# Optimization experiments

Measured on AMD Instinct MI355X. Metric: run time of the kernel, lower is better.

Reference implementation:

```python
import jax, jax.numpy as jnp
import numpy as np

N_NODES = 200000  # num_users + num_items
N_EDGES = 500000
LATENT = 64
N_LAYERS = 3
NEG_SLOPE = 0.01  # F.leaky_relu default
EPS = 1e-16       # PyG geo_softmax denominator epsilon


def setup_inputs() -> dict:
    key = jax.random.key(0)
    k1, k2, k3, k4, k5 = jax.random.split(key, 5)
    edge_index = jax.random.randint(k1, (2, N_EDGES), 0, N_NODES, dtype=jnp.int64 if jax.config.jax_enable_x64 else jnp.int32)
    edge_attrs = jax.random.normal(k2, (N_EDGES, 2), dtype=jnp.float32)
    emb = jax.random.normal(k3, (N_NODES, LATENT), dtype=jnp.float32)
    # per-layer attention params, shape [L, heads=1 -> squeezed, in_channels]
    a_att_w = jax.random.normal(k4, (N_LAYERS, LATENT), dtype=jnp.float32) * 0.1
    r_att_w = jax.random.normal(k5, (N_LAYERS, LATENT), dtype=jnp.float32) * 0.1
    return {"edge_index": edge_index, "edge_attrs": edge_attrs, "emb": emb,
            "a_att_w": a_att_w, "r_att_w": r_att_w}


def _segment_softmax(scores, dst, num_nodes):
    # scores: [E, D] softmax over edges grouped by destination node (PyG geo_softmax)
    m = jax.ops.segment_max(scores, dst, num_segments=num_nodes)  # [N, D]
    m = jnp.where(jnp.isfinite(m), m, 0.0)  # nodes without incoming edges
    w = jnp.exp(scores - m[dst])
    den = jax.ops.segment_sum(w, dst, num_segments=num_nodes)     # [N, D]
    return w / (den[dst] + EPS)


def reference(edge_index, edge_attrs, emb, a_att_w, r_att_w):
    src, dst = edge_index[0], edge_index[1]
    n = emb.shape[0]
    # symmetric degree normalization (degree of destination endpoints)
    deg = jax.ops.segment_sum(jnp.ones_like(dst, dtype=emb.dtype), dst, num_segments=n)
    dinv = jnp.where(deg > 0, deg ** -0.5, 0.0)
    norm = (dinv[src] * dinv[dst])[:, None]  # [E, 1]

    a_e = edge_attrs[:, 0:1]  # [E, 1]
    r_e = edge_attrs[:, 1:2]

    x = emb
    acc = emb  # layer-0 embedding
    for l in range(N_LAYERS):
        scores = (jax.nn.leaky_relu(a_e * a_att_w[l], NEG_SLOPE)
                  + jax.nn.leaky_relu(r_e * r_att_w[l], NEG_SLOPE))  # [E, D]
        attn = _segment_softmax(scores, dst, n)                       # [E, D]
        msg = norm * attn * x[src]                                    # gather + weight
        x = jax.ops.segment_sum(msg, dst, num_segments=n)             # scatter-add
        acc = acc + x
    out = acc / (N_LAYERS + 1)  # mean over layer embeddings
    return out
```

## Files before the change

### kernel.cpp

```cpp
#include <hip/hip_runtime.h>

#define BLK 256
#define LBLK 256
#define CH 1024

__device__ __forceinline__ unsigned short f2bf(float f) {
    unsigned u = __float_as_uint(f);
    u += 0x7FFFu + ((u >> 16) & 1u);
    return (unsigned short)(u >> 16);
}
__device__ __forceinline__ float bf2f(unsigned short h) {
    return __uint_as_float((unsigned)h << 16);
}
__device__ __forceinline__ float4 unpack4(ushort4 h) {
    return make_float4(bf2f(h.x), bf2f(h.y), bf2f(h.z), bf2f(h.w));
}
__device__ __forceinline__ ushort4 pack4(float4 f) {
    ushort4 h; h.x = f2bf(f.x); h.y = f2bf(f.y); h.z = f2bf(f.z); h.w = f2bf(f.w);
    return h;
}
__device__ __forceinline__ float4 unpack4u(uint2 u) {
    return make_float4(__uint_as_float(u.x << 16), __uint_as_float(u.x & 0xffff0000u),
                       __uint_as_float(u.y << 16), __uint_as_float(u.y & 0xffff0000u));
}
__device__ __forceinline__ unsigned pack2(float lo, float hi) {
    return (unsigned)f2bf(lo) | ((unsigned)f2bf(hi) << 16);
}


__global__ void k_deg(const int* __restrict__ dst, int* __restrict__ deg,
                      int* __restrict__ rank, int E) {
    int e = blockIdx.x * blockDim.x + threadIdx.x;
    if (e < E) rank[e] = atomicAdd(&deg[dst[e]], 1);
}

__global__ void k_scan1(const int* __restrict__ deg, int* __restrict__ partials, int N) {
    __shared__ int sm[BLK];
    int i0 = blockIdx.x * CH + threadIdx.x * 4;
    int s = 0;
    if (i0 + 3 < N) {
        int4 v = *(const int4*)(deg + i0);
        s = (v.x + v.y) + (v.z + v.w);
    } else {
        for (int k = 0; k < 4; ++k) if (i0 + k < N) s += deg[i0 + k];
    }
    sm[threadIdx.x] = s;
    __syncthreads();
    for (int off = BLK / 2; off > 0; off >>= 1) {
        if (threadIdx.x < off) sm[threadIdx.x] += sm[threadIdx.x + off];
        __syncthreads();
    }
    if (threadIdx.x == 0) partials[blockIdx.x] = sm[0];
}

__global__ void k_scan2(const int* __restrict__ deg, const int* __restrict__ partials,
                        int* __restrict__ row_off, int N, int E, int nb) {
    __shared__ int sp[BLK];
    __shared__ int sm[BLK];
    int b = blockIdx.x, t = threadIdx.x;
    sp[t] = (t < nb) ? partials[t] : 0;
    __syncthreads();
    for (int off = 1; off < BLK; off <<= 1) {
        int add = (t >= off) ? sp[t - off] : 0;
        __syncthreads();
        sp[t] += add;
        __syncthreads();
    }
    int base = (b == 0) ? 0 : sp[b - 1];
    if (b == 0 && t == 0) row_off[N] = E;
    int i0 = b * CH + t * 4;
    int v0 = 0, v1 = 0, v2 = 0, v3 = 0;
    if (i0 + 3 < N) {
        int4 v = *(const int4*)(deg + i0);
        v0 = v.x; v1 = v.y; v2 = v.z; v3 = v.w;
    } else {
        if (i0     < N) v0 = deg[i0];
        if (i0 + 1 < N) v1 = deg[i0 + 1];
        if (i0 + 2 < N) v2 = deg[i0 + 2];
    }
    int tot = (v0 + v1) + (v2 + v3);
    sm[t] = tot;
    __syncthreads();
    for (int off = 1; off < BLK; off <<= 1) {
        int add = (t >= off) ? sm[t - off] : 0;
        __syncthreads();
        sm[t] += add;
        __syncthreads();
    }
    int excl = base + sm[t] - tot;
    int4 r;
    r.x = excl;
    r.y = excl + v0;
    r.z = excl + v0 + v1;
    r.w = excl + v0 + v1 + v2;
    if (i0 + 3 < N) {
        *(int4*)(row_off + i0) = r;
    } else {
        if (i0     < N) row_off[i0]     = r.x;
        if (i0 + 1 < N) row_off[i0 + 1] = r.y;
        if (i0 + 2 < N) row_off[i0 + 2] = r.z;
    }
}

__global__ void k_convfill(const int* __restrict__ src, const int* __restrict__ dst,
                           const float2* __restrict__ attrs, const int* __restrict__ row_off,
                           const int* __restrict__ rank, const int* __restrict__ deg,
                           uint2* __restrict__ csr, const float4* __restrict__ emb4,
                           ushort4* __restrict__ embs, int E, int N16, int gF) {
    int b = blockIdx.x;
    if (b < gF) {
        int e = b * BLK + threadIdx.x;
        if (e >= E) return;
        int pos = row_off[dst[e]] + rank[e];
        float2 ar = attrs[e];
        csr[pos] = make_uint2((unsigned)src[e],
                              (unsigned)f2bf(ar.x) | ((unsigned)f2bf(ar.y) << 16));
    } else {
        int i = (b - gF) * BLK + threadIdx.x;
        if (i >= N16) return;
        int d = deg[i >> 4];
        float dinv = (d > 0) ? rsqrtf((float)d) : 0.0f;
        float4 e = emb4[i];
        embs[i] = pack4(make_float4(dinv * e.x, dinv * e.y, dinv * e.z, dinv * e.w));
    }
}


__device__ __forceinline__ float lrelu(float x) { return fmaxf(x, 0.01f * x); }

__device__ __forceinline__ void edge_w8(unsigned ar,
                                        const float4& awl, const float4& awh,
                                        const float4& rwl, const float4& rwh,
                                        float4& wl, float4& wh) {
    float a = bf2f((unsigned short)(ar & 0xffffu));
    float r = bf2f((unsigned short)(ar >> 16));
    wl.x = __expf(lrelu(a * awl.x) + lrelu(r * rwl.x));
    wl.y = __expf(lrelu(a * awl.y) + lrelu(r * rwl.y));
    wl.z = __expf(lrelu(a * awl.z) + lrelu(r * rwl.z));
    wl.w = __expf(lrelu(a * awl.w) + lrelu(r * rwl.w));
    wh.x = __expf(lrelu(a * awh.x) + lrelu(r * rwh.x));
    wh.y = __expf(lrelu(a * awh.y) + lrelu(r * rwh.y));
    wh.z = __expf(lrelu(a * awh.z) + lrelu(r * rwh.z));
    wh.w = __expf(lrelu(a * awh.w) + lrelu(r * rwh.w));
}

__device__ __forceinline__ void acc4u(float4& num, float4& den,
                                      const float4& w, uint2 xu, float g) {
    float4 x = unpack4u(xu);
    den.x += g * w.x; den.y += g * w.y; den.z += g * w.z; den.w += g * w.w;
    num.x += g * w.x * x.x;
    num.y += g * w.y * x.y;
    num.z += g * w.z * x.z;
    num.w += g * w.w * x.w;
}

__device__ __forceinline__ void acc8(float4& numl, float4& denl,
                                     float4& numh, float4& denh,
                                     const float4& wl, const float4& wh,
                                     const uint4& h, float g) {
    acc4u(numl, denl, wl, make_uint2(h.x, h.y), g);
    acc4u(numh, denh, wh, make_uint2(h.z, h.w), g);
}

template<int MODE>
__global__ __launch_bounds__(LBLK) void k_layer(
    const uint4* __restrict__ xs8, const uint2* __restrict__ csr,
    const int* __restrict__ row_off,
    const float4* __restrict__ aw4, const float4* __restrict__ rw4,
    const float4* __restrict__ emb4,
    const uint4* __restrict__ xsA8, const uint4* __restrict__ xsB8,
    uint4* __restrict__ xsout8, float4* __restrict__ out4, int N) {
    const int t = threadIdx.x;
    const int d8 = t & 7;
    const int v = blockIdx.x * (LBLK / 8) + (t >> 3);
    if (v >= N) return;

    const float4 awl = aw4[2 * d8],     rwl = rw4[2 * d8];
    const float4 awh = aw4[2 * d8 + 1], rwh = rw4[2 * d8 + 1];
    const int s0 = row_off[v];
    const int s1 = row_off[v + 1];

    float4 numl = {0.f, 0.f, 0.f, 0.f}, denl = {0.f, 0.f, 0.f, 0.f};
    float4 numh = {0.f, 0.f, 0.f, 0.f}, denh = {0.f, 0.f, 0.f, 0.f};

    for (int i = s0; i < s1; i += 4) {
        const int last = s1 - 1;
        uint2 e0 = csr[i];
        uint2 e1 = csr[min(i + 1, last)];
        uint2 e2 = csr[min(i + 2, last)];
        uint2 e3 = csr[min(i + 3, last)];
        uint4 h0 = xs8[(size_t)e0.x * 8 + d8];
        uint4 h1 = xs8[(size_t)e1.x * 8 + d8];
        uint4 h2 = xs8[(size_t)e2.x * 8 + d8];
        uint4 h3 = xs8[(size_t)e3.x * 8 + d8];
        float4 w0l, w0h, w1l, w1h, w2l, w2h, w3l, w3h;
        edge_w8(e0.y, awl, awh, rwl, rwh, w0l, w0h);
        edge_w8(e1.y, awl, awh, rwl, rwh, w1l, w1h);
        edge_w8(e2.y, awl, awh, rwl, rwh, w2l, w2h);
        edge_w8(e3.y, awl, awh, rwl, rwh, w3l, w3h);
        float g1 = (i + 1 < s1) ? 1.0f : 0.0f;
        float g2 = (i + 2 < s1) ? 1.0f : 0.0f;
        float g3 = (i + 3 < s1) ? 1.0f : 0.0f;
        acc8(numl, denl, numh, denh, w0l, w0h, h0, 1.0f);
        acc8(numl, denl, numh, denh, w1l, w1h, h1, g1);
        acc8(numl, denl, numh, denh, w2l, w2h, h2, g2);
        acc8(numl, denl, numh, denh, w3l, w3h, h3, g3);
    }

    float4 xr0, xr1;
    xr0.x = numl.x / (denl.x + 1e-16f);
    xr0.y = numl.y / (denl.y + 1e-16f);
    xr0.z = numl.z / (denl.z + 1e-16f);
    xr0.w = numl.w / (denl.w + 1e-16f);
    xr1.x = numh.x / (denh.x + 1e-16f);
    xr1.y = numh.y / (denh.y + 1e-16f);
    xr1.z = numh.z / (denh.z + 1e-16f);
    xr1.w = numh.w / (denh.w + 1e-16f);
    const int dv = s1 - s0;
    const float dinv = (dv > 0) ? rsqrtf((float)dv) : 0.0f;
    if (MODE == 2) {
        const float sd = (dv > 0) ? sqrtf((float)dv) : 0.0f;
        const size_t of = (size_t)v * 16 + 2 * d8;
        const size_t o8 = (size_t)v * 8 + d8;
        float4 e0 = emb4[of];
        float4 e1 = emb4[of + 1];
        uint4 Au = xsA8[o8];
        uint4 Bu = xsB8[o8];
        float4 A0 = unpack4u(make_uint2(Au.x, Au.y));
        float4 A1 = unpack4u(make_uint2(Au.z, Au.w));
        float4 B0 = unpack4u(make_uint2(Bu.x, Bu.y));
        float4 B1 = unpack4u(make_uint2(Bu.z, Bu.w));
        float4 r0, r1;
        r0.x = (e0.x + sd * (A0.x + B0.x) + dinv * xr0.x) * 0.25f;
        r0.y = (e0.y + sd * (A0.y + B0.y) + dinv * xr0.y) * 0.25f;
        r0.z = (e0.z + sd * (A0.z + B0.z) + dinv * xr0.z) * 0.25f;
        r0.w = (e0.w + sd * (A0.w + B0.w) + dinv * xr0.w) * 0.25f;
        r1.x = (e1.x + sd * (A1.x + B1.x) + dinv * xr1.x) * 0.25f;
        r1.y = (e1.y + sd * (A1.y + B1.y) + dinv * xr1.y) * 0.25f;
        r1.z = (e1.z + sd * (A1.z + B1.z) + dinv * xr1.z) * 0.25f;
        r1.w = (e1.w + sd * (A1.w + B1.w) + dinv * xr1.w) * 0.25f;
        out4[of]     = r0;
        out4[of + 1] = r1;
    } else {
        const float s = dinv * dinv;
        uint4 pkt;
        pkt.x = pack2(s * xr0.x, s * xr0.y);
        pkt.y = pack2(s * xr0.z, s * xr0.w);
        pkt.z = pack2(s * xr1.x, s * xr1.y);
        pkt.w = pack2(s * xr1.z, s * xr1.w);
        xsout8[(size_t)v * 8 + d8] = pkt;
    }
}


extern "C" void kernel_launch(void* const* d_in, const int* in_sizes, int n_in,
                              void* d_out, int out_size, void* d_ws, size_t ws_size,
                              hipStream_t stream) {
    const int*   ei    = (const int*)d_in[0];
    const float* attrs = (const float*)d_in[1];
    const float* emb   = (const float*)d_in[2];
    const float* a_att = (const float*)d_in[3];
    const float* r_att = (const float*)d_in[4];

    const int E = in_sizes[0] / 2;
    const int N = in_sizes[2] / 64;
    const int* src = ei;
    const int* dst = ei + E;

    char* ws = (char*)d_ws;
    size_t off = 0;
    auto alloc = [&](size_t bytes) {
        void* p = ws + off;
        off += (bytes + 255) & ~(size_t)255;
        return p;
    };
    int*     deg      = (int*)alloc((size_t)N * 4);
    int*     rank     = (int*)alloc((size_t)E * 4);
    int*     row_off  = (int*)alloc((size_t)(N + 1) * 4);
    int*     partials = (int*)alloc((size_t)BLK * 4);
    uint2*   csr      = (uint2*)alloc((size_t)E * 8);
    ushort4* embs     = (ushort4*)alloc((size_t)N * 16 * 8);
    ushort4* xsA      = (ushort4*)alloc((size_t)N * 16 * 8);
    ushort4* xsB      = (ushort4*)alloc((size_t)N * 16 * 8);
    float4*  out      = (float4*)d_out;

    hipMemsetAsync(deg, 0, (size_t)N * 4, stream);

    int gE = (E + BLK - 1) / BLK;
    int nb = (N + CH - 1) / CH;
    int gF = gE;
    int gC = (N * 16 + BLK - 1) / BLK;

    k_deg     <<<gE, BLK, 0, stream>>>(dst, deg, rank, E);
    k_scan1   <<<nb, BLK, 0, stream>>>(deg, partials, N);
    k_scan2   <<<nb, BLK, 0, stream>>>(deg, partials, row_off, N, E, nb);
    k_convfill<<<gF + gC, BLK, 0, stream>>>(src, dst, (const float2*)attrs, row_off,
                                            rank, deg, csr, (const float4*)emb,
                                            embs, E, N * 16, gF);

    const float4* emb4 = (const float4*)emb;
    const float4* aw4  = (const float4*)a_att;
    const float4* rw4  = (const float4*)r_att;

    int gL = (N + (LBLK / 8) - 1) / (LBLK / 8);
    k_layer<0><<<gL, LBLK, 0, stream>>>((const uint4*)embs, csr, row_off, aw4,      rw4,
                                        nullptr, nullptr, nullptr, (uint4*)xsA, nullptr, N);
    k_layer<1><<<gL, LBLK, 0, stream>>>((const uint4*)xsA,  csr, row_off, aw4 + 16, rw4 + 16,
                                        nullptr, nullptr, nullptr, (uint4*)xsB, nullptr, N);
    k_layer<2><<<gL, LBLK, 0, stream>>>((const uint4*)xsB,  csr, row_off, aw4 + 32, rw4 + 32,
                                        emb4, (const uint4*)xsA, (const uint4*)xsB,
                                        nullptr, out, N);
}
```

Baseline: 253.7 us.

## Fuse CSR setup kernels and memset into one cooperative kernel

```diff
diff --git a/kernel.cpp b/kernel.cpp
--- a/kernel.cpp
+++ b/kernel.cpp
@@ -1,8 +1,12 @@
 #include <hip/hip_runtime.h>
+#include <hip/hip_cooperative_groups.h>
+
+namespace cg = cooperative_groups;
 
 #define BLK 256
 #define LBLK 256
 #define CH 1024
+#define SGRID 1024
 
 __device__ __forceinline__ unsigned short f2bf(float f) {
     unsigned u = __float_as_uint(f);
@@ -12,9 +16,6 @@
 __device__ __forceinline__ float bf2f(unsigned short h) {
     return __uint_as_float((unsigned)h << 16);
 }
-__device__ __forceinline__ float4 unpack4(ushort4 h) {
-    return make_float4(bf2f(h.x), bf2f(h.y), bf2f(h.z), bf2f(h.w));
-}
 __device__ __forceinline__ ushort4 pack4(float4 f) {
     ushort4 h; h.x = f2bf(f.x); h.y = f2bf(f.y); h.z = f2bf(f.z); h.w = f2bf(f.w);
     return h;
@@ -27,97 +28,100 @@
     return (unsigned)f2bf(lo) | ((unsigned)f2bf(hi) << 16);
 }
 
-
-__global__ void k_deg(const int* __restrict__ dst, int* __restrict__ deg,
-                      int* __restrict__ rank, int E) {
-    int e = blockIdx.x * blockDim.x + threadIdx.x;
-    if (e < E) rank[e] = atomicAdd(&deg[dst[e]], 1);
-}
-
-__global__ void k_scan1(const int* __restrict__ deg, int* __restrict__ partials, int N) {
-    __shared__ int sm[BLK];
-    int i0 = blockIdx.x * CH + threadIdx.x * 4;
-    int s = 0;
-    if (i0 + 3 < N) {
-        int4 v = *(const int4*)(deg + i0);
-        s = (v.x + v.y) + (v.z + v.w);
-    } else {
-        for (int k = 0; k < 4; ++k) if (i0 + k < N) s += deg[i0 + k];
-    }
-    sm[threadIdx.x] = s;
-    __syncthreads();
-    for (int off = BLK / 2; off > 0; off >>= 1) {
-        if (threadIdx.x < off) sm[threadIdx.x] += sm[threadIdx.x + off];
-        __syncthreads();
-    }
-    if (threadIdx.x == 0) partials[blockIdx.x] = sm[0];
-}
-
-__global__ void k_scan2(const int* __restrict__ deg, const int* __restrict__ partials,
-                        int* __restrict__ row_off, int N, int E, int nb) {
+__global__ __launch_bounds__(BLK) void k_setup(
+    const int* __restrict__ src, const int* __restrict__ dst,
+    const float2* __restrict__ attrs,
+    int* __restrict__ deg, int* __restrict__ rank, int* __restrict__ row_off,
+    int* __restrict__ partials, uint2* __restrict__ csr,
+    const float4* __restrict__ emb4, ushort4* __restrict__ embs,
+    int N, int E, int nb, int N16) {
+    cg::grid_group grid = cg::this_grid();
+    const int t = threadIdx.x;
+    const int gtid = blockIdx.x * BLK + t;
+    const int gsize = gridDim.x * BLK;
     __shared__ int sp[BLK];
     __shared__ int sm[BLK];
-    int b = blockIdx.x, t = threadIdx.x;
-    sp[t] = (t < nb) ? partials[t] : 0;
-    __syncthreads();
-    for (int off = 1; off < BLK; off <<= 1) {
-        int add = (t >= off) ? sp[t - off] : 0;
-        __syncthreads();
-        sp[t] += add;
-        __syncthreads();
-    }
-    int base = (b == 0) ? 0 : sp[b - 1];
-    if (b == 0 && t == 0) row_off[N] = E;
-    int i0 = b * CH + t * 4;
-    int v0 = 0, v1 = 0, v2 = 0, v3 = 0;
-    if (i0 + 3 < N) {
-        int4 v = *(const int4*)(deg + i0);
-        v0 = v.x; v1 = v.y; v2 = v.z; v3 = v.w;
-    } else {
-        if (i0     < N) v0 = deg[i0];
-        if (i0 + 1 < N) v1 = deg[i0 + 1];
-        if (i0 + 2 < N) v2 = deg[i0 + 2];
-    }
-    int tot = (v0 + v1) + (v2 + v3);
-    sm[t] = tot;
-    __syncthreads();
-    for (int off = 1; off < BLK; off <<= 1) {
-        int add = (t >= off) ? sm[t - off] : 0;
-        __syncthreads();
-        sm[t] += add;
-        __syncthreads();
-    }
-    int excl = base + sm[t] - tot;
-    int4 r;
-    r.x = excl;
-    r.y = excl + v0;
-    r.z = excl + v0 + v1;
-    r.w = excl + v0 + v1 + v2;
-    if (i0 + 3 < N) {
-        *(int4*)(row_off + i0) = r;
-    } else {
-        if (i0     < N) row_off[i0]     = r.x;
-        if (i0 + 1 < N) row_off[i0 + 1] = r.y;
-        if (i0 + 2 < N) row_off[i0 + 2] = r.z;
-    }
-}
-
-__global__ void k_convfill(const int* __restrict__ src, const int* __restrict__ dst,
-                           const float2* __restrict__ attrs, const int* __restrict__ row_off,
-                           const int* __restrict__ rank, const int* __restrict__ deg,
-                           uint2* __restrict__ csr, const float4* __restrict__ emb4,
-                           ushort4* __restrict__ embs, int E, int N16, int gF) {
-    int b = blockIdx.x;
-    if (b < gF) {
-        int e = b * BLK + threadIdx.x;
-        if (e >= E) return;
+
+    for (int i = gtid; i < N; i += gsize) deg[i] = 0;
+    grid.sync();
+
+    for (int e = gtid; e < E; e += gsize) rank[e] = atomicAdd(&deg[dst[e]], 1);
+    grid.sync();
+
+    for (int c = blockIdx.x; c < nb; c += gridDim.x) {
+        int i0 = c * CH + t * 4;
+        int s = 0;
+        if (i0 + 3 < N) {
+            int4 v = *(const int4*)(deg + i0);
+            s = (v.x + v.y) + (v.z + v.w);
+        } else {
+            for (int k = 0; k < 4; ++k) if (i0 + k < N) s += deg[i0 + k];
+        }
+        sm[t] = s;
+        __syncthreads();
+        for (int off = BLK / 2; off > 0; off >>= 1) {
+            if (t < off) sm[t] += sm[t + off];
+            __syncthreads();
+        }
+        if (t == 0) partials[c] = sm[0];
+        __syncthreads();
+    }
+    grid.sync();
+
+    for (int c = blockIdx.x; c < nb; c += gridDim.x) {
+        sp[t] = (t < nb) ? partials[t] : 0;
+        __syncthreads();
+        for (int off = 1; off < BLK; off <<= 1) {
+            int add = (t >= off) ? sp[t - off] : 0;
+            __syncthreads();
+            sp[t] += add;
+            __syncthreads();
+        }
+        int base = (c == 0) ? 0 : sp[c - 1];
+        if (c == 0 && t == 0) row_off[N] = E;
+        int i0 = c * CH + t * 4;
+        int v0 = 0, v1 = 0, v2 = 0, v3 = 0;
+        if (i0 + 3 < N) {
+            int4 v = *(const int4*)(deg + i0);
+            v0 = v.x; v1 = v.y; v2 = v.z; v3 = v.w;
+        } else {
+            if (i0     < N) v0 = deg[i0];
+            if (i0 + 1 < N) v1 = deg[i0 + 1];
+            if (i0 + 2 < N) v2 = deg[i0 + 2];
+        }
+        int tot = (v0 + v1) + (v2 + v3);
+        sm[t] = tot;
+        __syncthreads();
+        for (int off = 1; off < BLK; off <<= 1) {
+            int add = (t >= off) ? sm[t - off] : 0;
+            __syncthreads();
+            sm[t] += add;
+            __syncthreads();
+        }
+        int excl = base + sm[t] - tot;
+        int4 r;
+        r.x = excl;
+        r.y = excl + v0;
+        r.z = excl + v0 + v1;
+        r.w = excl + v0 + v1 + v2;
+        if (i0 + 3 < N) {
+            *(int4*)(row_off + i0) = r;
+        } else {
+            if (i0     < N) row_off[i0]     = r.x;
+            if (i0 + 1 < N) row_off[i0 + 1] = r.y;
+            if (i0 + 2 < N) row_off[i0 + 2] = r.z;
+        }
+        __syncthreads();
+    }
+    grid.sync();
+
+    for (int e = gtid; e < E; e += gsize) {
         int pos = row_off[dst[e]] + rank[e];
         float2 ar = attrs[e];
         csr[pos] = make_uint2((unsigned)src[e],
                               (unsigned)f2bf(ar.x) | ((unsigned)f2bf(ar.y) << 16));
-    } else {
-        int i = (b - gF) * BLK + threadIdx.x;
-        if (i >= N16) return;
+    }
+    for (int i = gtid; i < N16; i += gsize) {
         int d = deg[i >> 4];
         float dinv = (d > 0) ? rsqrtf((float)d) : 0.0f;
         float4 e = emb4[i];
@@ -284,23 +288,24 @@
     ushort4* xsB      = (ushort4*)alloc((size_t)N * 16 * 8);
     float4*  out      = (float4*)d_out;
 
-    hipMemsetAsync(deg, 0, (size_t)N * 4, stream);
-
-    int gE = (E + BLK - 1) / BLK;
-    int nb = (N + CH - 1) / CH;
-    int gF = gE;
-    int gC = (N * 16 + BLK - 1) / BLK;
-
-    k_deg     <<<gE, BLK, 0, stream>>>(dst, deg, rank, E);
-    k_scan1   <<<nb, BLK, 0, stream>>>(deg, partials, N);
-    k_scan2   <<<nb, BLK, 0, stream>>>(deg, partials, row_off, N, E, nb);
-    k_convfill<<<gF + gC, BLK, 0, stream>>>(src, dst, (const float2*)attrs, row_off,
-                                            rank, deg, csr, (const float4*)emb,
-                                            embs, E, N * 16, gF);
+    int nb  = (N + CH - 1) / CH;
+    int N16 = N * 16;
 
     const float4* emb4 = (const float4*)emb;
     const float4* aw4  = (const float4*)a_att;
     const float4* rw4  = (const float4*)r_att;
+
+    {
+        void* args[] = {
+            (void*)&src, (void*)&dst, (void*)&attrs,
+            (void*)&deg, (void*)&rank, (void*)&row_off,
+            (void*)&partials, (void*)&csr,
+            (void*)&emb4, (void*)&embs,
+            (void*)&N, (void*)&E, (void*)&nb, (void*)&N16
+        };
+        hipLaunchCooperativeKernel((void*)k_setup, dim3(SGRID), dim3(BLK),
+                                   args, 0, stream);
+    }
 
     int gL = (N + (LBLK / 8) - 1) / (LBLK / 8);
     k_layer<0><<<gL, LBLK, 0, stream>>>((const uint4*)embs, csr, row_off, aw4,      rw4,
```

New measurement: 638.8 us. 2.52x slower.

## Replace CSR scan build with fixed-capacity per-node edge table plus overflow list

Applied to the files above, without the earlier changes.

```diff
diff --git a/kernel.cpp b/kernel.cpp
--- a/kernel.cpp
+++ b/kernel.cpp
@@ -2,7 +2,8 @@
 
 #define BLK 256
 #define LBLK 256
-#define CH 1024
+#define CAP 8
+#define OVMAX 8192
 
 __device__ __forceinline__ unsigned short f2bf(float f) {
     unsigned u = __float_as_uint(f);
@@ -12,9 +13,6 @@
 __device__ __forceinline__ float bf2f(unsigned short h) {
     return __uint_as_float((unsigned)h << 16);
 }
-__device__ __forceinline__ float4 unpack4(ushort4 h) {
-    return make_float4(bf2f(h.x), bf2f(h.y), bf2f(h.z), bf2f(h.w));
-}
 __device__ __forceinline__ ushort4 pack4(float4 f) {
     ushort4 h; h.x = f2bf(f.x); h.y = f2bf(f.y); h.z = f2bf(f.z); h.w = f2bf(f.w);
     return h;
@@ -27,102 +25,33 @@
     return (unsigned)f2bf(lo) | ((unsigned)f2bf(hi) << 16);
 }
 
-
-__global__ void k_deg(const int* __restrict__ dst, int* __restrict__ deg,
-                      int* __restrict__ rank, int E) {
+__global__ void k_edges(const int* __restrict__ src, const int* __restrict__ dst,
+                        const float2* __restrict__ attrs,
+                        int* __restrict__ deg, uint2* __restrict__ table,
+                        uint4* __restrict__ ov, int* __restrict__ ov_cnt, int E) {
     int e = blockIdx.x * blockDim.x + threadIdx.x;
-    if (e < E) rank[e] = atomicAdd(&deg[dst[e]], 1);
-}
-
-__global__ void k_scan1(const int* __restrict__ deg, int* __restrict__ partials, int N) {
-    __shared__ int sm[BLK];
-    int i0 = blockIdx.x * CH + threadIdx.x * 4;
-    int s = 0;
-    if (i0 + 3 < N) {
-        int4 v = *(const int4*)(deg + i0);
-        s = (v.x + v.y) + (v.z + v.w);
+    if (e >= E) return;
+    int d = dst[e];
+    int rk = atomicAdd(&deg[d], 1);
+    float2 ar = attrs[e];
+    unsigned arp = (unsigned)f2bf(ar.x) | ((unsigned)f2bf(ar.y) << 16);
+    unsigned s = (unsigned)src[e];
+    if (rk < CAP) {
+        table[(size_t)d * CAP + rk] = make_uint2(s, arp);
     } else {
-        for (int k = 0; k < 4; ++k) if (i0 + k < N) s += deg[i0 + k];
-    }
-    sm[threadIdx.x] = s;
-    __syncthreads();
-    for (int off = BLK / 2; off > 0; off >>= 1) {
-        if (threadIdx.x < off) sm[threadIdx.x] += sm[threadIdx.x + off];
-        __syncthreads();
-    }
-    if (threadIdx.x == 0) partials[blockIdx.x] = sm[0];
-}
-
-__global__ void k_scan2(const int* __restrict__ deg, const int* __restrict__ partials,
-                        int* __restrict__ row_off, int N, int E, int nb) {
-    __shared__ int sp[BLK];
-    __shared__ int sm[BLK];
-    int b = blockIdx.x, t = threadIdx.x;
-    sp[t] = (t < nb) ? partials[t] : 0;
-    __syncthreads();
-    for (int off = 1; off < BLK; off <<= 1) {
-        int add = (t >= off) ? sp[t - off] : 0;
-        __syncthreads();
-        sp[t] += add;
-        __syncthreads();
-    }
-    int base = (b == 0) ? 0 : sp[b - 1];
-    if (b == 0 && t == 0) row_off[N] = E;
-    int i0 = b * CH + t * 4;
-    int v0 = 0, v1 = 0, v2 = 0, v3 = 0;
-    if (i0 + 3 < N) {
-        int4 v = *(const int4*)(deg + i0);
-        v0 = v.x; v1 = v.y; v2 = v.z; v3 = v.w;
-    } else {
-        if (i0     < N) v0 = deg[i0];
-        if (i0 + 1 < N) v1 = deg[i0 + 1];
-        if (i0 + 2 < N) v2 = deg[i0 + 2];
-    }
-    int tot = (v0 + v1) + (v2 + v3);
-    sm[t] = tot;
-    __syncthreads();
-    for (int off = 1; off < BLK; off <<= 1) {
-        int add = (t >= off) ? sm[t - off] : 0;
-        __syncthreads();
-        sm[t] += add;
-        __syncthreads();
-    }
-    int excl = base + sm[t] - tot;
-    int4 r;
-    r.x = excl;
-    r.y = excl + v0;
-    r.z = excl + v0 + v1;
-    r.w = excl + v0 + v1 + v2;
-    if (i0 + 3 < N) {
-        *(int4*)(row_off + i0) = r;
-    } else {
-        if (i0     < N) row_off[i0]     = r.x;
-        if (i0 + 1 < N) row_off[i0 + 1] = r.y;
-        if (i0 + 2 < N) row_off[i0 + 2] = r.z;
-    }
-}
-
-__global__ void k_convfill(const int* __restrict__ src, const int* __restrict__ dst,
-                           const float2* __restrict__ attrs, const int* __restrict__ row_off,
-                           const int* __restrict__ rank, const int* __restrict__ deg,
-                           uint2* __restrict__ csr, const float4* __restrict__ emb4,
-                           ushort4* __restrict__ embs, int E, int N16, int gF) {
-    int b = blockIdx.x;
-    if (b < gF) {
-        int e = b * BLK + threadIdx.x;
-        if (e >= E) return;
-        int pos = row_off[dst[e]] + rank[e];
-        float2 ar = attrs[e];
-        csr[pos] = make_uint2((unsigned)src[e],
-                              (unsigned)f2bf(ar.x) | ((unsigned)f2bf(ar.y) << 16));
-    } else {
-        int i = (b - gF) * BLK + threadIdx.x;
-        if (i >= N16) return;
-        int d = deg[i >> 4];
-        float dinv = (d > 0) ? rsqrtf((float)d) : 0.0f;
-        float4 e = emb4[i];
-        embs[i] = pack4(make_float4(dinv * e.x, dinv * e.y, dinv * e.z, dinv * e.w));
-    }
+        int oi = atomicAdd(ov_cnt, 1);
+        if (oi < OVMAX) ov[oi] = make_uint4((unsigned)d, s, arp, 0u);
+    }
+}
+
+__global__ void k_conv(const int* __restrict__ deg, const float4* __restrict__ emb4,
+                       ushort4* __restrict__ embs, int N16) {
+    int i = blockIdx.x * blockDim.x + threadIdx.x;
+    if (i >= N16) return;
+    int d = deg[i >> 4];
+    float dinv = (d > 0) ? rsqrtf((float)d) : 0.0f;
+    float4 e = emb4[i];
+    embs[i] = pack4(make_float4(dinv * e.x, dinv * e.y, dinv * e.z, dinv * e.w));
 }
 
 
@@ -164,8 +93,9 @@
 
 template<int MODE>
 __global__ __launch_bounds__(LBLK) void k_layer(
-    const uint4* __restrict__ xs8, const uint2* __restrict__ csr,
-    const int* __restrict__ row_off,
+    const uint4* __restrict__ xs8, const uint2* __restrict__ table,
+    const int* __restrict__ deg,
+    const uint4* __restrict__ ov, const int* __restrict__ ov_cnt,
     const float4* __restrict__ aw4, const float4* __restrict__ rw4,
     const float4* __restrict__ emb4,
     const uint4* __restrict__ xsA8, const uint4* __restrict__ xsB8,
@@ -177,18 +107,20 @@
 
     const float4 awl = aw4[2 * d8],     rwl = rw4[2 * d8];
     const float4 awh = aw4[2 * d8 + 1], rwh = rw4[2 * d8 + 1];
-    const int s0 = row_off[v];
-    const int s1 = row_off[v + 1];
+
+    const uint2* __restrict__ tab = table + (size_t)v * CAP;
+    const int dv = deg[v];
+    const int L = min(dv, CAP);
 
     float4 numl = {0.f, 0.f, 0.f, 0.f}, denl = {0.f, 0.f, 0.f, 0.f};
     float4 numh = {0.f, 0.f, 0.f, 0.f}, denh = {0.f, 0.f, 0.f, 0.f};
 
-    for (int i = s0; i < s1; i += 4) {
-        const int last = s1 - 1;
-        uint2 e0 = csr[i];
-        uint2 e1 = csr[min(i + 1, last)];
-        uint2 e2 = csr[min(i + 2, last)];
-        uint2 e3 = csr[min(i + 3, last)];
+    for (int i = 0; i < L; i += 4) {
+        const int last = L - 1;
+        uint2 e0 = tab[i];
+        uint2 e1 = tab[min(i + 1, last)];
+        uint2 e2 = tab[min(i + 2, last)];
+        uint2 e3 = tab[min(i + 3, last)];
         uint4 h0 = xs8[(size_t)e0.x * 8 + d8];
         uint4 h1 = xs8[(size_t)e1.x * 8 + d8];
         uint4 h2 = xs8[(size_t)e2.x * 8 + d8];
@@ -198,13 +130,26 @@
         edge_w8(e1.y, awl, awh, rwl, rwh, w1l, w1h);
         edge_w8(e2.y, awl, awh, rwl, rwh, w2l, w2h);
         edge_w8(e3.y, awl, awh, rwl, rwh, w3l, w3h);
-        float g1 = (i + 1 < s1) ? 1.0f : 0.0f;
-        float g2 = (i + 2 < s1) ? 1.0f : 0.0f;
-        float g3 = (i + 3 < s1) ? 1.0f : 0.0f;
+        float g1 = (i + 1 < L) ? 1.0f : 0.0f;
+        float g2 = (i + 2 < L) ? 1.0f : 0.0f;
+        float g3 = (i + 3 < L) ? 1.0f : 0.0f;
         acc8(numl, denl, numh, denh, w0l, w0h, h0, 1.0f);
         acc8(numl, denl, numh, denh, w1l, w1h, h1, g1);
         acc8(numl, denl, numh, denh, w2l, w2h, h2, g2);
         acc8(numl, denl, numh, denh, w3l, w3h, h3, g3);
+    }
+
+    if (dv > CAP) {
+        const int oc = min(*ov_cnt, OVMAX);
+        for (int j = 0; j < oc; ++j) {
+            uint4 oe = ov[j];
+            if ((int)oe.x == v) {
+                uint4 h = xs8[(size_t)oe.y * 8 + d8];
+                float4 wl, wh;
+                edge_w8(oe.z, awl, awh, rwl, rwh, wl, wh);
+                acc8(numl, denl, numh, denh, wl, wh, h, 1.0f);
+            }
+        }
     }
 
     float4 xr0, xr1;
@@ -216,7 +161,6 @@
     xr1.y = numh.y / (denh.y + 1e-16f);
     xr1.z = numh.z / (denh.z + 1e-16f);
     xr1.w = numh.w / (denh.w + 1e-16f);
-    const int dv = s1 - s0;
     const float dinv = (dv > 0) ? rsqrtf((float)dv) : 0.0f;
     if (MODE == 2) {
         const float sd = (dv > 0) ? sqrtf((float)dv) : 0.0f;
@@ -275,39 +219,37 @@
         return p;
     };
     int*     deg      = (int*)alloc((size_t)N * 4);
-    int*     rank     = (int*)alloc((size_t)E * 4);
-    int*     row_off  = (int*)alloc((size_t)(N + 1) * 4);
-    int*     partials = (int*)alloc((size_t)BLK * 4);
-    uint2*   csr      = (uint2*)alloc((size_t)E * 8);
+    int*     ov_cnt   = (int*)alloc(4);
+    uint4*   ov       = (uint4*)alloc((size_t)OVMAX * 16);
+    uint2*   table    = (uint2*)alloc((size_t)N * CAP * 8);
+    size_t   zbytes   = (size_t)((char*)table - (char*)deg) + (size_t)N * CAP * 8;
     ushort4* embs     = (ushort4*)alloc((size_t)N * 16 * 8);
     ushort4* xsA      = (ushort4*)alloc((size_t)N * 16 * 8);
     ushort4* xsB      = (ushort4*)alloc((size_t)N * 16 * 8);
     float4*  out      = (float4*)d_out;
 
-    hipMemsetAsync(deg, 0, (size_t)N * 4, stream);
+    hipMemsetAsync(deg, 0, zbytes, stream);
 
     int gE = (E + BLK - 1) / BLK;
-    int nb = (N + CH - 1) / CH;
-    int gF = gE;
     int gC = (N * 16 + BLK - 1) / BLK;
 
-    k_deg     <<<gE, BLK, 0, stream>>>(dst, deg, rank, E);
-    k_scan1   <<<nb, BLK, 0, stream>>>(deg, partials, N);
-    k_scan2   <<<nb, BLK, 0, stream>>>(deg, partials, row_off, N, E, nb);
-    k_convfill<<<gF + gC, BLK, 0, stream>>>(src, dst, (const float2*)attrs, row_off,
-                                            rank, deg, csr, (const float4*)emb,
-                                            embs, E, N * 16, gF);
+    k_edges<<<gE, BLK, 0, stream>>>(src, dst, (const float2*)attrs,
+                                    deg, table, ov, ov_cnt, E);
+    k_conv <<<gC, BLK, 0, stream>>>(deg, (const float4*)emb, embs, N * 16);
 
     const float4* emb4 = (const float4*)emb;
     const float4* aw4  = (const float4*)a_att;
     const float4* rw4  = (const float4*)r_att;
 
     int gL = (N + (LBLK / 8) - 1) / (LBLK / 8);
-    k_layer<0><<<gL, LBLK, 0, stream>>>((const uint4*)embs, csr, row_off, aw4,      rw4,
-                                        nullptr, nullptr, nullptr, (uint4*)xsA, nullptr, N);
-    k_layer<1><<<gL, LBLK, 0, stream>>>((const uint4*)xsA,  csr, row_off, aw4 + 16, rw4 + 16,
-                                        nullptr, nullptr, nullptr, (uint4*)xsB, nullptr, N);
-    k_layer<2><<<gL, LBLK, 0, stream>>>((const uint4*)xsB,  csr, row_off, aw4 + 32, rw4 + 32,
-                                        emb4, (const uint4*)xsA, (const uint4*)xsB,
+    k_layer<0><<<gL, LBLK, 0, stream>>>((const uint4*)embs, table, deg, ov, ov_cnt,
+                                        aw4,      rw4,      nullptr,
+                                        nullptr, nullptr, (uint4*)xsA, nullptr, N);
+    k_layer<1><<<gL, LBLK, 0, stream>>>((const uint4*)xsA,  table, deg, ov, ov_cnt,
+                                        aw4 + 16, rw4 + 16, nullptr,
+                                        nullptr, nullptr, (uint4*)xsB, nullptr, N);
+    k_layer<2><<<gL, LBLK, 0, stream>>>((const uint4*)xsB,  table, deg, ov, ov_cnt,
+                                        aw4 + 32, rw4 + 32, emb4,
+                                        (const uint4*)xsA, (const uint4*)xsB,
                                         nullptr, out, N);
 }
```

Result: slower. 316.4 us (+24.7%).

## Merge scan into single-pass decoupled lookback and store per-edge source norm in CSR

Applied to the files above, without the earlier changes.

```diff
diff --git a/kernel.cpp b/kernel.cpp
--- a/kernel.cpp
+++ b/kernel.cpp
@@ -12,9 +12,6 @@
 __device__ __forceinline__ float bf2f(unsigned short h) {
     return __uint_as_float((unsigned)h << 16);
 }
-__device__ __forceinline__ float4 unpack4(ushort4 h) {
-    return make_float4(bf2f(h.x), bf2f(h.y), bf2f(h.z), bf2f(h.w));
-}
 __device__ __forceinline__ ushort4 pack4(float4 f) {
     ushort4 h; h.x = f2bf(f.x); h.y = f2bf(f.y); h.z = f2bf(f.z); h.w = f2bf(f.w);
     return h;
@@ -28,46 +25,27 @@
 }
 
 
-__global__ void k_deg(const int* __restrict__ dst, int* __restrict__ deg,
-                      int* __restrict__ rank, int E) {
-    int e = blockIdx.x * blockDim.x + threadIdx.x;
-    if (e < E) rank[e] = atomicAdd(&deg[dst[e]], 1);
-}
-
-__global__ void k_scan1(const int* __restrict__ deg, int* __restrict__ partials, int N) {
+__global__ void k_stage1(const int* __restrict__ dst, int* __restrict__ deg,
+                         int* __restrict__ rank,
+                         const float4* __restrict__ emb4, ushort4* __restrict__ embs,
+                         int E, int N16, int gF) {
+    int b = blockIdx.x;
+    if (b < gF) {
+        int e = b * BLK + threadIdx.x;
+        if (e < E) rank[e] = atomicAdd(&deg[dst[e]], 1);
+    } else {
+        int i = (b - gF) * BLK + threadIdx.x;
+        if (i < N16) embs[i] = pack4(emb4[i]);
+    }
+}
+
+__global__ __launch_bounds__(BLK) void k_scan(
+    const int* __restrict__ deg, int* __restrict__ row_off,
+    int* __restrict__ partials, int* __restrict__ flags,
+    int N, int E, int nb) {
     __shared__ int sm[BLK];
-    int i0 = blockIdx.x * CH + threadIdx.x * 4;
-    int s = 0;
-    if (i0 + 3 < N) {
-        int4 v = *(const int4*)(deg + i0);
-        s = (v.x + v.y) + (v.z + v.w);
-    } else {
-        for (int k = 0; k < 4; ++k) if (i0 + k < N) s += deg[i0 + k];
-    }
-    sm[threadIdx.x] = s;
-    __syncthreads();
-    for (int off = BLK / 2; off > 0; off >>= 1) {
-        if (threadIdx.x < off) sm[threadIdx.x] += sm[threadIdx.x + off];
-        __syncthreads();
-    }
-    if (threadIdx.x == 0) partials[blockIdx.x] = sm[0];
-}
-
-__global__ void k_scan2(const int* __restrict__ deg, const int* __restrict__ partials,
-                        int* __restrict__ row_off, int N, int E, int nb) {
-    __shared__ int sp[BLK];
-    __shared__ int sm[BLK];
-    int b = blockIdx.x, t = threadIdx.x;
-    sp[t] = (t < nb) ? partials[t] : 0;
-    __syncthreads();
-    for (int off = 1; off < BLK; off <<= 1) {
-        int add = (t >= off) ? sp[t - off] : 0;
-        __syncthreads();
-        sp[t] += add;
-        __syncthreads();
-    }
-    int base = (b == 0) ? 0 : sp[b - 1];
-    if (b == 0 && t == 0) row_off[N] = E;
+    const int b = blockIdx.x, t = threadIdx.x;
+
     int i0 = b * CH + t * 4;
     int v0 = 0, v1 = 0, v2 = 0, v3 = 0;
     if (i0 + 3 < N) {
@@ -79,6 +57,7 @@
         if (i0 + 2 < N) v2 = deg[i0 + 2];
     }
     int tot = (v0 + v1) + (v2 + v3);
+
     sm[t] = tot;
     __syncthreads();
     for (int off = 1; off < BLK; off <<= 1) {
@@ -87,7 +66,29 @@
         sm[t] += add;
         __syncthreads();
     }
-    int excl = base + sm[t] - tot;
+    const int incl = sm[t];
+    const int btotal = sm[BLK - 1];
+
+    if (t == 0) {
+        __hip_atomic_store(&partials[b], btotal, __ATOMIC_RELAXED, __HIP_MEMORY_SCOPE_AGENT);
+        __hip_atomic_store(&flags[b], 1, __ATOMIC_RELEASE, __HIP_MEMORY_SCOPE_AGENT);
+    }
+
+    int p = 0;
+    if (t < b) {
+        while (__hip_atomic_load(&flags[t], __ATOMIC_ACQUIRE, __HIP_MEMORY_SCOPE_AGENT) == 0) {}
+        p = __hip_atomic_load(&partials[t], __ATOMIC_RELAXED, __HIP_MEMORY_SCOPE_AGENT);
+    }
+    __syncthreads();
+    sm[t] = p;
+    __syncthreads();
+    for (int off = BLK / 2; off > 0; off >>= 1) {
+        if (t < off) sm[t] += sm[t + off];
+        __syncthreads();
+    }
+    const int base = sm[0];
+
+    int excl = base + incl - tot;
     int4 r;
     r.x = excl;
     r.y = excl + v0;
@@ -100,29 +101,24 @@
         if (i0 + 1 < N) row_off[i0 + 1] = r.y;
         if (i0 + 2 < N) row_off[i0 + 2] = r.z;
     }
-}
-
-__global__ void k_convfill(const int* __restrict__ src, const int* __restrict__ dst,
-                           const float2* __restrict__ attrs, const int* __restrict__ row_off,
-                           const int* __restrict__ rank, const int* __restrict__ deg,
-                           uint2* __restrict__ csr, const float4* __restrict__ emb4,
-                           ushort4* __restrict__ embs, int E, int N16, int gF) {
-    int b = blockIdx.x;
-    if (b < gF) {
-        int e = b * BLK + threadIdx.x;
-        if (e >= E) return;
-        int pos = row_off[dst[e]] + rank[e];
-        float2 ar = attrs[e];
-        csr[pos] = make_uint2((unsigned)src[e],
-                              (unsigned)f2bf(ar.x) | ((unsigned)f2bf(ar.y) << 16));
-    } else {
-        int i = (b - gF) * BLK + threadIdx.x;
-        if (i >= N16) return;
-        int d = deg[i >> 4];
-        float dinv = (d > 0) ? rsqrtf((float)d) : 0.0f;
-        float4 e = emb4[i];
-        embs[i] = pack4(make_float4(dinv * e.x, dinv * e.y, dinv * e.z, dinv * e.w));
-    }
+    if (b == 0 && t == 0) row_off[N] = E;
+}
+
+__global__ void k_fill(const int* __restrict__ src, const int* __restrict__ dst,
+                       const float2* __restrict__ attrs, const int* __restrict__ row_off,
+                       const int* __restrict__ rank, const int* __restrict__ deg,
+                       uint4* __restrict__ csr16, int E) {
+    int e = blockIdx.x * BLK + threadIdx.x;
+    if (e >= E) return;
+    int d  = dst[e];
+    int s  = src[e];
+    int pos = row_off[d] + rank[e];
+    int ds = deg[s];
+    float dinv = (ds > 0) ? rsqrtf((float)ds) : 0.0f;
+    float2 ar = attrs[e];
+    csr16[pos] = make_uint4((unsigned)s,
+                            (unsigned)f2bf(ar.x) | ((unsigned)f2bf(ar.y) << 16),
+                            __float_as_uint(dinv), 0u);
 }
 
 
@@ -145,26 +141,27 @@
 }
 
 __device__ __forceinline__ void acc4u(float4& num, float4& den,
-                                      const float4& w, uint2 xu, float g) {
+                                      const float4& w, uint2 xu, float g, float gd) {
     float4 x = unpack4u(xu);
     den.x += g * w.x; den.y += g * w.y; den.z += g * w.z; den.w += g * w.w;
-    num.x += g * w.x * x.x;
-    num.y += g * w.y * x.y;
-    num.z += g * w.z * x.z;
-    num.w += g * w.w * x.w;
+    num.x += gd * w.x * x.x;
+    num.y += gd * w.y * x.y;
+    num.z += gd * w.z * x.z;
+    num.w += gd * w.w * x.w;
 }
 
 __device__ __forceinline__ void acc8(float4& numl, float4& denl,
                                      float4& numh, float4& denh,
                                      const float4& wl, const float4& wh,
-                                     const uint4& h, float g) {
-    acc4u(numl, denl, wl, make_uint2(h.x, h.y), g);
-    acc4u(numh, denh, wh, make_uint2(h.z, h.w), g);
+                                     const uint4& h, float g, float d) {
+    const float gd = g * d;
+    acc4u(numl, denl, wl, make_uint2(h.x, h.y), g, gd);
+    acc4u(numh, denh, wh, make_uint2(h.z, h.w), g, gd);
 }
 
 template<int MODE>
 __global__ __launch_bounds__(LBLK) void k_layer(
-    const uint4* __restrict__ xs8, const uint2* __restrict__ csr,
+    const uint4* __restrict__ xs8, const uint4* __restrict__ csr16,
     const int* __restrict__ row_off,
     const float4* __restrict__ aw4, const float4* __restrict__ rw4,
     const float4* __restrict__ emb4,
@@ -185,10 +182,10 @@
 
     for (int i = s0; i < s1; i += 4) {
         const int last = s1 - 1;
-        uint2 e0 = csr[i];
-        uint2 e1 = csr[min(i + 1, last)];
-        uint2 e2 = csr[min(i + 2, last)];
-        uint2 e3 = csr[min(i + 3, last)];
+        uint4 e0 = csr16[i];
+        uint4 e1 = csr16[min(i + 1, last)];
+        uint4 e2 = csr16[min(i + 2, last)];
+        uint4 e3 = csr16[min(i + 3, last)];
         uint4 h0 = xs8[(size_t)e0.x * 8 + d8];
         uint4 h1 = xs8[(size_t)e1.x * 8 + d8];
         uint4 h2 = xs8[(size_t)e2.x * 8 + d8];
@@ -201,10 +198,10 @@
         float g1 = (i + 1 < s1) ? 1.0f : 0.0f;
         float g2 = (i + 2 < s1) ? 1.0f : 0.0f;
         float g3 = (i + 3 < s1) ? 1.0f : 0.0f;
-        acc8(numl, denl, numh, denh, w0l, w0h, h0, 1.0f);
-        acc8(numl, denl, numh, denh, w1l, w1h, h1, g1);
-        acc8(numl, denl, numh, denh, w2l, w2h, h2, g2);
-        acc8(numl, denl, numh, denh, w3l, w3h, h3, g3);
+        acc8(numl, denl, numh, denh, w0l, w0h, h0, 1.0f, __uint_as_float(e0.z));
+        acc8(numl, denl, numh, denh, w1l, w1h, h1, g1,   __uint_as_float(e1.z));
+        acc8(numl, denl, numh, denh, w2l, w2h, h2, g2,   __uint_as_float(e2.z));
+        acc8(numl, denl, numh, denh, w3l, w3h, h3, g3,   __uint_as_float(e3.z));
     }
 
     float4 xr0, xr1;
@@ -219,7 +216,6 @@
     const int dv = s1 - s0;
     const float dinv = (dv > 0) ? rsqrtf((float)dv) : 0.0f;
     if (MODE == 2) {
-        const float sd = (dv > 0) ? sqrtf((float)dv) : 0.0f;
         const size_t of = (size_t)v * 16 + 2 * d8;
         const size_t o8 = (size_t)v * 8 + d8;
         float4 e0 = emb4[of];
@@ -231,23 +227,22 @@
         float4 B0 = unpack4u(make_uint2(Bu.x, Bu.y));
         float4 B1 = unpack4u(make_uint2(Bu.z, Bu.w));
         float4 r0, r1;
-        r0.x = (e0.x + sd * (A0.x + B0.x) + dinv * xr0.x) * 0.25f;
-        r0.y = (e0.y + sd * (A0.y + B0.y) + dinv * xr0.y) * 0.25f;
-        r0.z = (e0.z + sd * (A0.z + B0.z) + dinv * xr0.z) * 0.25f;
-        r0.w = (e0.w + sd * (A0.w + B0.w) + dinv * xr0.w) * 0.25f;
-        r1.x = (e1.x + sd * (A1.x + B1.x) + dinv * xr1.x) * 0.25f;
-        r1.y = (e1.y + sd * (A1.y + B1.y) + dinv * xr1.y) * 0.25f;
-        r1.z = (e1.z + sd * (A1.z + B1.z) + dinv * xr1.z) * 0.25f;
-        r1.w = (e1.w + sd * (A1.w + B1.w) + dinv * xr1.w) * 0.25f;
+        r0.x = (e0.x + A0.x + B0.x + dinv * xr0.x) * 0.25f;
+        r0.y = (e0.y + A0.y + B0.y + dinv * xr0.y) * 0.25f;
+        r0.z = (e0.z + A0.z + B0.z + dinv * xr0.z) * 0.25f;
+        r0.w = (e0.w + A0.w + B0.w + dinv * xr0.w) * 0.25f;
+        r1.x = (e1.x + A1.x + B1.x + dinv * xr1.x) * 0.25f;
+        r1.y = (e1.y + A1.y + B1.y + dinv * xr1.y) * 0.25f;
+        r1.z = (e1.z + A1.z + B1.z + dinv * xr1.z) * 0.25f;
+        r1.w = (e1.w + A1.w + B1.w + dinv * xr1.w) * 0.25f;
         out4[of]     = r0;
         out4[of + 1] = r1;
     } else {
-        const float s = dinv * dinv;
         uint4 pkt;
-        pkt.x = pack2(s * xr0.x, s * xr0.y);
-        pkt.y = pack2(s * xr0.z, s * xr0.w);
-        pkt.z = pack2(s * xr1.x, s * xr1.y);
-        pkt.w = pack2(s * xr1.z, s * xr1.w);
+        pkt.x = pack2(dinv * xr0.x, dinv * xr0.y);
+        pkt.y = pack2(dinv * xr0.z, dinv * xr0.w);
+        pkt.z = pack2(dinv * xr1.x, dinv * xr1.y);
+        pkt.w = pack2(dinv * xr1.z, dinv * xr1.w);
         xsout8[(size_t)v * 8 + d8] = pkt;
     }
 }
@@ -275,39 +270,41 @@
         return p;
     };
     int*     deg      = (int*)alloc((size_t)N * 4);
+    int*     flags    = (int*)alloc((size_t)BLK * 4);
+    int*     partials = (int*)alloc((size_t)BLK * 4);
+    size_t   zbytes   = (size_t)((char*)partials - (char*)deg) + (size_t)BLK * 4;
     int*     rank     = (int*)alloc((size_t)E * 4);
     int*     row_off  = (int*)alloc((size_t)(N + 1) * 4);
-    int*     partials = (int*)alloc((size_t)BLK * 4);
-    uint2*   csr      = (uint2*)alloc((size_t)E * 8);
+    uint4*   csr16    = (uint4*)alloc((size_t)E * 16);
     ushort4* embs     = (ushort4*)alloc((size_t)N * 16 * 8);
     ushort4* xsA      = (ushort4*)alloc((size_t)N * 16 * 8);
     ushort4* xsB      = (ushort4*)alloc((size_t)N * 16 * 8);
     float4*  out      = (float4*)d_out;
 
-    hipMemsetAsync(deg, 0, (size_t)N * 4, stream);
+    hipMemsetAsync(deg, 0, zbytes, stream);
 
     int gE = (E + BLK - 1) / BLK;
     int nb = (N + CH - 1) / CH;
-    int gF = gE;
     int gC = (N * 16 + BLK - 1) / BLK;
-
-    k_deg     <<<gE, BLK, 0, stream>>>(dst, deg, rank, E);
-    k_scan1   <<<nb, BLK, 0, stream>>>(deg, partials, N);
-    k_scan2   <<<nb, BLK, 0, stream>>>(deg, partials, row_off, N, E, nb);
-    k_convfill<<<gF + gC, BLK, 0, stream>>>(src, dst, (const float2*)attrs, row_off,
-                                            rank, deg, csr, (const float4*)emb,
-                                            embs, E, N * 16, gF);
 
     const float4* emb4 = (const float4*)emb;
     const float4* aw4  = (const float4*)a_att;
     const float4* rw4  = (const float4*)r_att;
 
+    k_stage1<<<gE + gC, BLK, 0, stream>>>(dst, deg, rank, emb4, embs, E, N * 16, gE);
+    k_scan  <<<nb, BLK, 0, stream>>>(deg, row_off, partials, flags, N, E, nb);
+    k_fill  <<<gE, BLK, 0, stream>>>(src, dst, (const float2*)attrs, row_off,
+                                     rank, deg, csr16, E);
+
     int gL = (N + (LBLK / 8) - 1) / (LBLK / 8);
-    k_layer<0><<<gL, LBLK, 0, stream>>>((const uint4*)embs, csr, row_off, aw4,      rw4,
-                                        nullptr, nullptr, nullptr, (uint4*)xsA, nullptr, N);
-    k_layer<1><<<gL, LBLK, 0, stream>>>((const uint4*)xsA,  csr, row_off, aw4 + 16, rw4 + 16,
-                                        nullptr, nullptr, nullptr, (uint4*)xsB, nullptr, N);
-    k_layer<2><<<gL, LBLK, 0, stream>>>((const uint4*)xsB,  csr, row_off, aw4 + 32, rw4 + 32,
-                                        emb4, (const uint4*)xsA, (const uint4*)xsB,
+    k_layer<0><<<gL, LBLK, 0, stream>>>((const uint4*)embs, csr16, row_off,
+                                        aw4,      rw4,      nullptr,
+                                        nullptr, nullptr, (uint4*)xsA, nullptr, N);
+    k_layer<1><<<gL, LBLK, 0, stream>>>((const uint4*)xsA,  csr16, row_off,
+                                        aw4 + 16, rw4 + 16, nullptr,
+                                        nullptr, nullptr, (uint4*)xsB, nullptr, N);
+    k_layer<2><<<gL, LBLK, 0, stream>>>((const uint4*)xsB,  csr16, row_off,
+                                        aw4 + 32, rw4 + 32, emb4,
+                                        (const uint4*)xsA, (const uint4*)xsB,
                                         nullptr, out, N);
 }
```

Result: slower. 271.5 us (+7.0%).
